# Kernel tuning notes

Measured on AMD Instinct MI355X. Metric: run time of the kernel, lower is better.

The kernel has to match this reference:

```python
import jax, jax.numpy as jnp
import numpy as np

HEADS, DH, DIM = 16, 64, 1024
GAMMA, LAMBDA_REG = 0.01, 0.001


def _ln(x, g, b, eps=1e-5):
    mu = x.mean(-1, keepdims=True)
    var = x.var(-1, keepdims=True)  # biased var, matches torch LayerNorm
    return (x - mu) / jnp.sqrt(var + eps) * g + b


def setup_inputs() -> dict:
    key = jax.random.key(0)
    ks = jax.random.split(key, 8)
    B, NQ, NK = 8, 512, 512
    inner = HEADS * DH
    rn = lambda i, shp, sc: jax.random.normal(ks[i], shp, jnp.float32) * sc
    return {
        "q": rn(0, (B, NQ, DIM), 1.0),
        "k": rn(1, (B, NK, DIM), 1.0),
        "v": rn(2, (B, NK, DIM), 1.0),
        "ln_g": jnp.ones((DIM,), jnp.float32),
        "ln_b": jnp.zeros((DIM,), jnp.float32),
        "w_in": rn(3, (DIM, inner), 0.02),
        "wp_w1": rn(4, (2 * DH, DH), 0.05),
        "wp_b1": jnp.zeros((DH,), jnp.float32),
        "wp_lng": jnp.ones((DH,), jnp.float32),
        "wp_lnb": jnp.zeros((DH,), jnp.float32),
        "wp_w2": rn(5, (DH, DH // 2), 0.05),
        "wp_b2": jnp.zeros((DH // 2,), jnp.float32),
        "wp_w3": rn(6, (DH // 2, 3), 0.05),
        "wp_b3": jnp.zeros((3,), jnp.float32),
        "w_temp": jnp.ones((1,), jnp.float32) * 0.8,
        "w_out": rn(7, (inner, DIM), 0.02),
        "b_out": jnp.zeros((DIM,), jnp.float32),
    }


def reference(q, k, v, ln_g, ln_b, w_in, wp_w1, wp_b1, wp_lng, wp_lnb,
              wp_w2, wp_b2, wp_w3, wp_b3, w_temp, w_out, b_out):
    sg = jax.lax.stop_gradient

    def proj(x):  # input_linear (dropout=identity in eval) + head split
        y = _ln(x, ln_g, ln_b) @ w_in                      # [B,N,inner]
        B, N, _ = y.shape
        return y.reshape(B, N, HEADS, DH).transpose(2, 0, 1, 3)  # [h,B,N,d]

    f_q, f_k, f_v = proj(q), proj(k), proj(v)
    m = f_k.shape[2]
    eps = 1e-8

    # --- cosine component (clamp applied twice, as in source) ---
    dots = jnp.einsum('hbnd,hbmd->hbnm', f_q, f_k)
    n1 = jnp.linalg.norm(f_q, axis=-1, keepdims=True) + eps   # [h,B,Nq,1]
    n2 = jnp.linalg.norm(f_k, axis=-1, keepdims=True) + eps   # [h,B,Nk,1]
    cosine_sim = jnp.clip(dots / (n1 * jnp.swapaxes(n2, -1, -2)), -0.98, 0.98)

    # --- regularized covariance component ---
    f_kc = f_k - f_k.mean(axis=2, keepdims=True)
    f_qc = f_q - f_q.mean(axis=-1, keepdims=True)
    cov = jnp.einsum('hbnd,hbmd->hbnm', f_qc, f_kc) / (DH ** 0.5 + 1e-6)
    health = jnp.std(cov, ddof=1)
    base = LAMBDA_REG / max(m, 1)
    reg = jnp.where(health < 1e-5, base * 5.0,
                    jnp.where(health < 1e-3, base * 2.0, base))
    cov = jnp.clip(reg * cov, -25.0, 25.0)

    # --- margin-based variance component (eval: adaptive_gamma = gamma) ---
    fqn = f_q / jnp.maximum(jnp.linalg.norm(f_q, axis=-1, keepdims=True), 1e-6)
    fkn = f_k / jnp.maximum(jnp.linalg.norm(f_k, axis=-1, keepdims=True), 1e-6)
    cs = jnp.clip(jnp.einsum('hbnd,hbmd->hbnm', fqn, fkn), -0.98, 0.98)
    margin = jnp.clip(GAMMA - cs, 0.0, 5.0)
    var_c = jnp.broadcast_to(margin.mean(-1, keepdims=True), cs.shape)

    # --- dynamic per-head weight predictor MLP ---
    qk = jnp.concatenate([f_q.mean(axis=(1, 2)), f_k.mean(axis=(1, 2))], -1)  # [h,2d]
    h1 = jax.nn.relu(_ln(qk @ wp_w1 + wp_b1, wp_lng, wp_lnb))
    h2 = jax.nn.relu(h1 @ wp_w2 + wp_b2)
    logits = jax.nn.softmax(h2 @ wp_w3 + wp_b3, -1)  # MLP ends in Softmax
    temp = jnp.clip(w_temp, 0.1, 5.0)
    w = jax.nn.softmax(logits / temp, -1)            # second softmax with temp
    w = jnp.clip(w, 0.08, 0.75)
    w = w / w.sum(-1, keepdims=True)
    cw = w[:, 0].reshape(HEADS, 1, 1, 1)
    covw = w[:, 1].reshape(HEADS, 1, 1, 1)
    varw = w[:, 2].reshape(HEADS, 1, 1, 1)

    # --- health-based normalization (stds detached, as in source) ---
    cn = sg(jnp.std(cosine_sim, ddof=1)) + 1e-6
    covn = sg(jnp.std(cov, ddof=1)) + 1e-6
    varn = sg(jnp.std(var_c, ddof=1)) + 1e-6
    ch = jnp.minimum(cn, 1.0)
    covh = jnp.minimum(covn * 10.0, 1.0)
    varh = jnp.minimum(varn * 10.0, 1.0)
    dots_f = (cw * (cosine_sim / cn * ch)
              + covw * (cov / covn * 0.4 * covh)
              + varw * (var_c / varn * 0.4 * varh))

    # --- diversity-adaptive softmax temperature ---
    div = jnp.std(dots_f, ddof=1)
    atemp = jnp.where(div < 1e-5, 0.05, jnp.where(div < 1e-3, 0.2, 0.5 + div))
    atemp = jnp.clip(atemp, 0.05, 2.0)
    attn = jax.nn.softmax(dots_f / atemp, axis=-1)

    out = jnp.einsum('hbnm,hbmd->hbnd', attn, f_v)
    out = out.transpose(1, 2, 0, 3).reshape(q.shape[0], q.shape[1], HEADS * DH)
    return out @ w_out + b_out  # output_linear (dropout=identity)
```

## Files before the change

### kernel.cpp

```cpp
#include <hip/hip_runtime.h>
#include <math.h>

#define NHEADS 16
#define DHEAD  64
#define NDIM   1024
#define NB     8
#define NSEQ   512
#define NROWS  4096
#define NHB    128
#define NTOTD  33554432.0

typedef __bf16 bf16x8 __attribute__((ext_vector_type(8)));
typedef __bf16 bf16x4 __attribute__((ext_vector_type(4)));
typedef float  f32x4  __attribute__((ext_vector_type(4)));

#define MFMA(a,b,c) __builtin_amdgcn_mfma_f32_16x16x32_bf16(a,b,c,0,0,0)

static __device__ __forceinline__ size_t qk_off(int hbq, int n, int d){
  return ((size_t)hbq*32 + (n>>4))*1024 + (size_t)(d>>3)*128 + (size_t)(n&15)*8 + (d&7);
}

#define O_DSUMH  0
#define O_DSUME  1024
#define O_SCAL   2048
#define O_COEF   3072
#define O_W      4096
#define O_RQ1    131072
#define O_RQ2    393216
#define O_MQ     655360
#define O_QDMK   917504
#define O_RK1    1179648
#define O_RK2    1441792
#define O_KS2    1703936
#define O_MARG   1966080
#define O_RCS    2228224
#define O_RCOV   2490368
#define O_MK     2752512
#define O_QCOL   2785280
#define O_QHI    4194304
#define O_QLO    12582912
#define O_KHI    20971520
#define O_KLO    29360128
#define O_VTH    37748736
#define O_VTL    46137344
#define O_LNST   54525952
#define O_WTH    71303168
#define O_WTL    73400320
#define O_OUTH   75497472
#define O_OUTL   83886080
#define O_WOTH   92274688
#define O_WOTL   94371840

static __device__ __forceinline__ float clamp98(float x){ return fminf(fmaxf(x,-0.98f),0.98f); }

__global__ __launch_bounds__(256) void ln_stats_kernel(const float* __restrict__ q,
    const float* __restrict__ k, const float* __restrict__ v, float* __restrict__ st){
  int row = blockIdx.x, t = threadIdx.x;
  const float* x = (blockIdx.y==0) ? q : (blockIdx.y==1 ? k : v);
  float4 vv = *(const float4*)(x + (size_t)row*1024 + t*4);
  float s  = vv.x+vv.y+vv.z+vv.w;
  float ss = vv.x*vv.x+vv.y*vv.y+vv.z*vv.z+vv.w*vv.w;
  for (int off=32; off; off>>=1){ s += __shfl_down(s,off); ss += __shfl_down(ss,off); }
  __shared__ float sh[8];
  if ((t&63)==0){ sh[t>>6]=s; sh[4+(t>>6)]=ss; }
  __syncthreads();
  if (t==0){
    float S=sh[0]+sh[1]+sh[2]+sh[3], SS=sh[4]+sh[5]+sh[6]+sh[7];
    float mu = S*(1.0f/1024.0f);
    st[blockIdx.y*8192 + row*2]   = mu;
    st[blockIdx.y*8192 + row*2+1] = 1.0f/sqrtf(SS*(1.0f/1024.0f) - mu*mu + 1e-5f);
  }
}

__global__ __launch_bounds__(256) void transpose_split_kernel(const float* __restrict__ wsrc,
    __bf16* __restrict__ th, __bf16* __restrict__ tl){
  __shared__ float tile[64][65];
  int k0 = blockIdx.x*64, n0 = blockIdx.y*64;
  int t = threadIdx.x;
  int c = t&63, r4 = t>>6;
  #pragma unroll
  for (int i=0;i<16;i++){
    int kr = r4 + i*4;
    tile[kr][c] = wsrc[(size_t)(k0+kr)*1024 + n0 + c];
  }
  __syncthreads();
  #pragma unroll
  for (int i=0;i<16;i++){
    int nr = r4 + i*4;
    float v = tile[c][nr];
    __bf16 hv = (__bf16)v;
    size_t o = (size_t)(n0+nr)*1024 + k0 + c;
    th[o] = hv; tl[o] = (__bf16)(v - (float)hv);
  }
}

__global__ __launch_bounds__(256) void proj_gemm_kernel(
  const float* __restrict__ q, const float* __restrict__ k, const float* __restrict__ v,
  const float* __restrict__ lnst0,
  const float* __restrict__ gv, const float* __restrict__ bv,
  const __bf16* __restrict__ Bth, const __bf16* __restrict__ Btl,
  __bf16* __restrict__ qhi, __bf16* __restrict__ qlo,
  __bf16* __restrict__ khi, __bf16* __restrict__ klo,
  __bf16* __restrict__ vth, __bf16* __restrict__ vtl)
{
  __shared__ __bf16 Ash[128][72];
  __shared__ __bf16 Asl[128][72];
  __shared__ __bf16 Bsh[64][72];
  __shared__ __bf16 Bsl[64][72];
  int z = blockIdx.z;
  const float* X = (z==0)? q : (z==1? k : v);
  const float* lnst = lnst0 + z*8192;
  __bf16* oh = (z==0)? qhi : (z==1? khi : vth);
  __bf16* ol = (z==0)? qlo : (z==1? klo : vtl);
  int t = threadIdx.x, w = t>>6, lane = t&63, lr = lane&15, lq = lane>>4;
  int vid = blockIdx.y*16 + blockIdx.x;
  int cX = vid&7, r2 = vid>>3;
  int ytile = cX*4 + (r2>>4);
  int xtile = r2&15;
  int rbase = ytile*128;
  int cbase = xtile*64;
  int wr = w>>1, wc = w&1;
  int srow = t>>3;
  int scol = (t&7)*8;
  f32x4 acc[4][2] = {};
  for (int kt=0; kt<16; kt++){
    int k0 = kt*64;
    bf16x8 va[4], vA[4], vb[2], vB[2];
    float4 g0 = *(const float4*)(gv + k0 + scol);
    float4 g1 = *(const float4*)(gv + k0 + scol + 4);
    float4 b0 = *(const float4*)(bv + k0 + scol);
    float4 b1 = *(const float4*)(bv + k0 + scol + 4);
    #pragma unroll
    for (int r=0;r<4;r++){
      int row = rbase + r*32 + srow;
      size_t gi = (size_t)row*1024 + k0 + scol;
      float4 x0 = *(const float4*)(X + gi);
      float4 x1 = *(const float4*)(X + gi + 4);
      float mu = lnst[row*2], rs = lnst[row*2+1];
      float o[8];
      o[0]=(x0.x-mu)*rs*g0.x+b0.x; o[1]=(x0.y-mu)*rs*g0.y+b0.y;
      o[2]=(x0.z-mu)*rs*g0.z+b0.z; o[3]=(x0.w-mu)*rs*g0.w+b0.w;
      o[4]=(x1.x-mu)*rs*g1.x+b1.x; o[5]=(x1.y-mu)*rs*g1.y+b1.y;
      o[6]=(x1.z-mu)*rs*g1.z+b1.z; o[7]=(x1.w-mu)*rs*g1.w+b1.w;
      bf16x8 hv, lv;
      #pragma unroll
      for (int e=0;e<8;e++){
        __bf16 hb_ = (__bf16)o[e];
        hv[e] = hb_; lv[e] = (__bf16)(o[e]-(float)hb_);
      }
      va[r]=hv; vA[r]=lv;
    }
    #pragma unroll
    for (int r=0;r<2;r++){
      size_t gi = (size_t)(cbase + r*32 + srow)*1024 + k0 + scol;
      vb[r] = *(const bf16x8*)(Bth + gi);
      vB[r] = *(const bf16x8*)(Btl + gi);
    }
    #pragma unroll
    for (int r=0;r<4;r++){
      *(bf16x8*)&Ash[r*32+srow][scol] = va[r];
      *(bf16x8*)&Asl[r*32+srow][scol] = vA[r];
    }
    #pragma unroll
    for (int r=0;r<2;r++){
      *(bf16x8*)&Bsh[r*32+srow][scol] = vb[r];
      *(bf16x8*)&Bsl[r*32+srow][scol] = vB[r];
    }
    __syncthreads();
    #pragma unroll
    for (int kc=0; kc<2; kc++){
      int ko = kc*32 + lq*8;
      bf16x8 ah[4], al[4], bh[2], bl[2];
      #pragma unroll
      for (int i=0;i<4;i++){
        ah[i] = *(const bf16x8*)&Ash[wr*64 + i*16 + lr][ko];
        al[i] = *(const bf16x8*)&Asl[wr*64 + i*16 + lr][ko];
      }
      #pragma unroll
      for (int j=0;j<2;j++){
        bh[j] = *(const bf16x8*)&Bsh[wc*32 + j*16 + lr][ko];
        bl[j] = *(const bf16x8*)&Bsl[wc*32 + j*16 + lr][ko];
      }
      #pragma unroll
      for (int i=0;i<4;i++)
        #pragma unroll
        for (int j=0;j<2;j++){
          acc[i][j] = MFMA(al[i], bh[j], acc[i][j]);
          acc[i][j] = MFMA(ah[i], bl[j], acc[i][j]);
          acc[i][j] = MFMA(ah[i], bh[j], acc[i][j]);
        }
    }
    __syncthreads();
  }
  #pragma unroll
  for (int i=0;i<4;i++)
    #pragma unroll
    for (int j=0;j<2;j++)
      #pragma unroll
      for (int r=0;r<4;r++){
        int row = rbase + wr*64 + i*16 + lq*4 + r;
        int col = cbase + wc*32 + j*16 + lr;
        float val = acc[i][j][r];
        __bf16 hv = (__bf16)val;
        __bf16 lv = (__bf16)(val - (float)hv);
        int n = row & 511, b2 = row >> 9;
        int hh = col >> 6, d = col & 63;
        int hbq = hh*8 + b2;
        size_t o;
        if (z<2){
          o = qk_off(hbq, n, d);
        } else {
          o = (((size_t)hbq*4 + (d>>4))*16 + (n>>5))*512
            + (size_t)((((n>>3)&3)*16) + (d&15))*8 + (n&7);
        }
        oh[o] = hv; ol[o] = lv;
      }
}

__global__ __launch_bounds__(256) void final_gemm_kernel(
  const __bf16* __restrict__ Ah, const __bf16* __restrict__ Al,
  const __bf16* __restrict__ Bth, const __bf16* __restrict__ Btl,
  const float* __restrict__ bias, float* __restrict__ of)
{
  __shared__ __bf16 Ash[128][72];
  __shared__ __bf16 Asl[128][72];
  __shared__ __bf16 Bsh[64][72];
  __shared__ __bf16 Bsl[64][72];
  int t = threadIdx.x, w = t>>6, lane = t&63, lr = lane&15, lq = lane>>4;
  int vid = blockIdx.y*16 + blockIdx.x;
  int cX = vid&7, r2 = vid>>3;
  int ytile = cX*4 + (r2>>4);
  int xtile = r2&15;
  int rbase = ytile*128;
  int cbase = xtile*64;
  int wr = w>>1, wc = w&1;
  int srow = t>>3;
  int scol = (t&7)*8;
  f32x4 acc[4][2] = {};
  for (int kt=0; kt<16; kt++){
    int k0 = kt*64;
    bf16x8 va[4], vA[4], vb[2], vB[2];
    #pragma unroll
    for (int r=0;r<4;r++){
      size_t gi = (size_t)(rbase + r*32 + srow)*1024 + k0 + scol;
      va[r] = *(const bf16x8*)(Ah + gi);
      vA[r] = *(const bf16x8*)(Al + gi);
    }
    #pragma unroll
    for (int r=0;r<2;r++){
      size_t gi = (size_t)(cbase + r*32 + srow)*1024 + k0 + scol;
      vb[r] = *(const bf16x8*)(Bth + gi);
      vB[r] = *(const bf16x8*)(Btl + gi);
    }
    #pragma unroll
    for (int r=0;r<4;r++){
      *(bf16x8*)&Ash[r*32+srow][scol] = va[r];
      *(bf16x8*)&Asl[r*32+srow][scol] = vA[r];
    }
    #pragma unroll
    for (int r=0;r<2;r++){
      *(bf16x8*)&Bsh[r*32+srow][scol] = vb[r];
      *(bf16x8*)&Bsl[r*32+srow][scol] = vB[r];
    }
    __syncthreads();
    #pragma unroll
    for (int kc=0; kc<2; kc++){
      int ko = kc*32 + lq*8;
      bf16x8 ah[4], al[4], bh[2], bl[2];
      #pragma unroll
      for (int i=0;i<4;i++){
        ah[i] = *(const bf16x8*)&Ash[wr*64 + i*16 + lr][ko];
        al[i] = *(const bf16x8*)&Asl[wr*64 + i*16 + lr][ko];
      }
      #pragma unroll
      for (int j=0;j<2;j++){
        bh[j] = *(const bf16x8*)&Bsh[wc*32 + j*16 + lr][ko];
        bl[j] = *(const bf16x8*)&Bsl[wc*32 + j*16 + lr][ko];
      }
      #pragma unroll
      for (int i=0;i<4;i++)
        #pragma unroll
        for (int j=0;j<2;j++){
          acc[i][j] = MFMA(al[i], bh[j], acc[i][j]);
          acc[i][j] = MFMA(ah[i], bl[j], acc[i][j]);
          acc[i][j] = MFMA(ah[i], bh[j], acc[i][j]);
        }
    }
    __syncthreads();
  }
  #pragma unroll
  for (int i=0;i<4;i++)
    #pragma unroll
    for (int j=0;j<2;j++)
      #pragma unroll
      for (int r=0;r<4;r++){
        int row = rbase + wr*64 + i*16 + lq*4 + r;
        int col = cbase + wc*32 + j*16 + lr;
        of[(size_t)row*1024 + col] = acc[i][j][r] + bias[col];
      }
}

__global__ void kstats_kernel(const __bf16* __restrict__ kh, const __bf16* __restrict__ kl,
    float* __restrict__ mk, float* __restrict__ rk1, float* __restrict__ rk2, float* __restrict__ ks2){
  int hb = blockIdx.x;
  size_t base = (size_t)hb*32768;
  int t = threadIdx.x;
  __shared__ float csA[32][64];
  __shared__ float mks_lds[64];
  __shared__ float mksum_sh;
  int c2 = t&7, mg = t>>3;
  float fs[8] = {};
  for (int m=mg; m<512; m+=32){
    size_t off = base + (size_t)(m>>4)*1024 + c2*128 + (size_t)(m&15)*8;
    bf16x8 h = *(const bf16x8*)(kh+off);
    bf16x8 l = *(const bf16x8*)(kl+off);
    #pragma unroll
    for (int e=0;e<8;e++) fs[e] += (float)h[e]+(float)l[e];
  }
  #pragma unroll
  for (int e=0;e<8;e++) csA[mg][c2*8+e] = fs[e];
  __syncthreads();
  if (t<64){
    float s=0;
    #pragma unroll
    for (int g=0;g<32;g++) s += csA[g][t];
    float vv = s*(1.0f/512.0f);
    mk[hb*64+t] = vv;
    mks_lds[t] = vv;
  }
  __syncthreads();
  if (t==0){
    float s=0;
    for (int i=0;i<64;i++) s += mks_lds[i];
    mksum_sh = s;
  }
  __syncthreads();
  float mks = mksum_sh;
  int l8 = t&7, rg = t>>3;
  for (int m=rg; m<512; m+=32){
    size_t off = base + (size_t)(m>>4)*1024 + l8*128 + (size_t)(m&15)*8;
    bf16x8 h = *(const bf16x8*)(kh+off);
    bf16x8 l = *(const bf16x8*)(kl+off);
    float s=0, ss=0;
    #pragma unroll
    for (int e=0;e<8;e++){ float vv=(float)h[e]+(float)l[e]; s+=vv; ss+=vv*vv; }
    for (int o2=4;o2;o2>>=1){ s+=__shfl_xor(s,o2); ss+=__shfl_xor(ss,o2); }
    if (l8==0){
      float nk = sqrtf(ss);
      rk1[hb*512+m] = 1.0f/(nk+1e-8f);
      rk2[hb*512+m] = 1.0f/fmaxf(nk,1e-6f);
      ks2[hb*512+m] = s - mks;
    }
  }
}

__global__ void qstats_kernel(const __bf16* __restrict__ qh, const __bf16* __restrict__ ql,
    const float* __restrict__ mk, float* __restrict__ rq1, float* __restrict__ rq2,
    float* __restrict__ mq, float* __restrict__ qdotmk, float* __restrict__ qcol){
  int hb = blockIdx.x;
  size_t base = (size_t)hb*32768;
  int t = threadIdx.x;
  __shared__ float csA[32][64];
  __shared__ float mks_lds[64];
  int c2 = t&7, mg = t>>3;
  if (t<64) mks_lds[t] = mk[hb*64+t];
  float fs[8] = {};
  for (int m=mg; m<512; m+=32){
    size_t off = base + (size_t)(m>>4)*1024 + c2*128 + (size_t)(m&15)*8;
    bf16x8 h = *(const bf16x8*)(qh+off);
    bf16x8 l = *(const bf16x8*)(ql+off);
    #pragma unroll
    for (int e=0;e<8;e++) fs[e] += (float)h[e]+(float)l[e];
  }
  #pragma unroll
  for (int e=0;e<8;e++) csA[mg][c2*8+e] = fs[e];
  __syncthreads();
  if (t<64){
    float s=0;
    #pragma unroll
    for (int g=0;g<32;g++) s += csA[g][t];
    qcol[hb*64+t] = s;
  }
  int l8 = t&7, rg = t>>3;
  float mkv[8];
  #pragma unroll
  for (int e=0;e<8;e++) mkv[e] = mks_lds[l8*8+e];
  for (int n=rg; n<512; n+=32){
    size_t off = base + (size_t)(n>>4)*1024 + l8*128 + (size_t)(n&15)*8;
    bf16x8 h = *(const bf16x8*)(qh+off);
    bf16x8 l = *(const bf16x8*)(ql+off);
    float s=0, ss=0, qd=0;
    #pragma unroll
    for (int e=0;e<8;e++){
      float vv=(float)h[e]+(float)l[e];
      s+=vv; ss+=vv*vv; qd+=vv*mkv[e];
    }
    for (int o2=4;o2;o2>>=1){ s+=__shfl_xor(s,o2); ss+=__shfl_xor(ss,o2); qd+=__shfl_xor(qd,o2); }
    if (l8==0){
      float nq = sqrtf(ss);
      rq1[hb*512+n] = 1.0f/(nq+1e-8f);
      rq2[hb*512+n] = 1.0f/fmaxf(nq,1e-6f);
      mq[hb*512+n]  = s*(1.0f/64.0f);
      qdotmk[hb*512+n] = qd;
    }
  }
}

__global__ void mlp_kernel(const float* __restrict__ qcol, const float* __restrict__ mk,
   const float* __restrict__ w1, const float* __restrict__ b1, const float* __restrict__ lng,
   const float* __restrict__ lnb, const float* __restrict__ w2, const float* __restrict__ b2,
   const float* __restrict__ w3, const float* __restrict__ b3, const float* __restrict__ wtemp,
   float* __restrict__ W){
  int h = blockIdx.x;
  int j = threadIdx.x;
  __shared__ float qk[128], h1[64], h2[32];
  float sq=0, sk=0;
  #pragma unroll
  for (int b=0;b<8;b++){
    sq += qcol[(h*8+b)*64 + j];
    sk += mk[(h*8+b)*64 + j];
  }
  qk[j]    = sq*(1.0f/4096.0f);
  qk[64+j] = sk*(1.0f/8.0f);
  __syncthreads();
  float a = b1[j];
  for (int i=0;i<128;i++) a += qk[i]*w1[i*64+j];
  float s=a, ss=a*a;
  for (int off=32; off; off>>=1){ s += __shfl_xor(s,off); ss += __shfl_xor(ss,off); }
  float mu = s*(1.0f/64.0f), var = ss*(1.0f/64.0f)-mu*mu;
  float v = (a-mu)/sqrtf(var+1e-5f)*lng[j] + lnb[j];
  h1[j] = fmaxf(v, 0.0f);
  __syncthreads();
  if (j<32){
    float a2 = b2[j];
    for (int i=0;i<64;i++) a2 += h1[i]*w2[i*32+j];
    h2[j] = fmaxf(a2,0.0f);
  }
  __syncthreads();
  if (j==0){
    float l[3];
    for (int kq=0;kq<3;kq++){ float a3=b3[kq]; for(int i=0;i<32;i++) a3 += h2[i]*w3[i*3+kq]; l[kq]=a3; }
    float m = fmaxf(l[0],fmaxf(l[1],l[2]));
    float e0=expf(l[0]-m), e1=expf(l[1]-m), e2=expf(l[2]-m);
    float si = 1.0f/(e0+e1+e2);
    float temp = fminf(fmaxf(wtemp[0], 0.1f), 5.0f);
    float t0=e0*si/temp, t1=e1*si/temp, t2=e2*si/temp;
    float m2 = fmaxf(t0,fmaxf(t1,t2));
    float f0=expf(t0-m2), f1=expf(t1-m2), f2=expf(t2-m2);
    float s2i = 1.0f/(f0+f1+f2);
    float wv[3] = {f0*s2i, f1*s2i, f2*s2i};
    float wsum=0.0f;
    for (int kq=0;kq<3;kq++){ wv[kq]=fminf(fmaxf(wv[kq],0.08f),0.75f); wsum+=wv[kq]; }
    for (int kq=0;kq<3;kq++) W[h*3+kq] = wv[kq]/wsum;
  }
}

__global__ __launch_bounds__(256) void s1_mfma_kernel(
  const __bf16* __restrict__ qhp, const __bf16* __restrict__ qlp,
  const __bf16* __restrict__ khp, const __bf16* __restrict__ klp,
  const float* __restrict__ rq1, const float* __restrict__ rq2,
  const float* __restrict__ mq, const float* __restrict__ qdmk,
  const float* __restrict__ rk1, const float* __restrict__ rk2,
  const float* __restrict__ ks2,
  double* __restrict__ dsumH, float* __restrict__ margin,
  float* __restrict__ rcs, float* __restrict__ rcov)
{
  int vid = blockIdx.y*4 + blockIdx.x;
  int cX = vid&7, r2 = vid>>3;
  int hb = cX*16 + (r2>>2);
  int n0 = (r2&3)*128;
  size_t qb = (size_t)hb*32768;
  __shared__ float sm[512][3];
  __shared__ float sn[128][4];
  int t = threadIdx.x;
  for (int mm=t; mm<512; mm+=256){
    int m = hb*512 + mm;
    sm[mm][0]=rk1[m]; sm[mm][1]=rk2[m]; sm[mm][2]=ks2[m];
  }
  if (t<128){
    int n = hb*512 + n0 + t;
    sn[t][0]=rq1[n]; sn[t][1]=rq2[n]; sn[t][2]=mq[n]; sn[t][3]=qdmk[n];
  }
  __syncthreads();
  int w = t>>6, lane = t&63, lr = lane&15, lq = lane>>4;
  int nw = w*32;
  float lcs=0,lcs2=0,lcov=0,lcov2=0,lcscov=0;
  float mrow[2][4]={}, csr[2][4]={}, cvr[2][4]={};
  for (int mc=0; mc<4; mc++){
    int m0 = mc*128;
    f32x4 acc[2][8] = {};
    #pragma unroll
    for (int kc=0; kc<2; kc++){
      bf16x8 ah[2], al[2];
      #pragma unroll
      for (int i=0;i<2;i++){
        size_t off = qb + (size_t)(((n0+nw)>>4)+i)*1024 + kc*512 + (size_t)lane*8;
        ah[i] = *(const bf16x8*)(qhp + off);
        al[i] = *(const bf16x8*)(qlp + off);
      }
      #pragma unroll
      for (int j=0;j<8;j++){
        size_t off = qb + (size_t)((m0>>4)+j)*1024 + kc*512 + (size_t)lane*8;
        bf16x8 bh = *(const bf16x8*)(khp + off);
        bf16x8 bl = *(const bf16x8*)(klp + off);
        #pragma unroll
        for (int i=0;i<2;i++){
          acc[i][j] = MFMA(ah[i], bh, acc[i][j]);
          acc[i][j] = MFMA(ah[i], bl, acc[i][j]);
          acc[i][j] = MFMA(al[i], bh, acc[i][j]);
        }
      }
    }
    #pragma unroll
    for (int i=0;i<2;i++){
      float nr1[4],nr2[4],nmq[4],nqd[4];
      #pragma unroll
      for (int r=0;r<4;r++){
        int nl = nw + i*16 + lq*4 + r;
        nr1[r]=sn[nl][0]; nr2[r]=sn[nl][1]; nmq[r]=sn[nl][2]; nqd[r]=sn[nl][3];
      }
      #pragma unroll
      for (int j=0;j<8;j++){
        int ml = m0 + j*16 + lr;
        float k1=sm[ml][0], k2=sm[ml][1], ksv=sm[ml][2];
        #pragma unroll
        for (int r=0;r<4;r++){
          float dv = acc[i][j][r];
          float cs = clamp98(dv*nr1[r]*k1);
          float c2 = clamp98(dv*nr2[r]*k2);
          float mg = fminf(fmaxf(0.01f-c2,0.0f),5.0f);
          float cv = dv - nqd[r] - nmq[r]*ksv;
          lcs+=cs; lcs2+=cs*cs; lcov+=cv; lcov2+=cv*cv; lcscov+=cs*cv;
          mrow[i][r]+=mg; csr[i][r]+=cs; cvr[i][r]+=cv;
        }
      }
    }
  }
  for (int off=1; off<16; off<<=1)
    #pragma unroll
    for (int i=0;i<2;i++)
      #pragma unroll
      for (int r=0;r<4;r++){
        mrow[i][r]+=__shfl_xor(mrow[i][r],off);
        csr[i][r] +=__shfl_xor(csr[i][r],off);
        cvr[i][r]+=__shfl_xor(cvr[i][r],off);
      }
  if (lr==0){
    #pragma unroll
    for (int i=0;i<2;i++)
      #pragma unroll
      for (int r=0;r<4;r++){
        int n = hb*512 + n0 + nw + i*16 + lq*4 + r;
        margin[n] = mrow[i][r]*(1.0f/512.0f);
        rcs[n]    = csr[i][r];
        rcov[n]   = cvr[i][r];
      }
  }
  for (int off=32; off; off>>=1){
    lcs+=__shfl_xor(lcs,off); lcs2+=__shfl_xor(lcs2,off);
    lcov+=__shfl_xor(lcov,off); lcov2+=__shfl_xor(lcov2,off);
    lcscov+=__shfl_xor(lcscov,off);
  }
  __shared__ double red[4][5];
  if (lane==0){ red[w][0]=lcs; red[w][1]=lcs2; red[w][2]=lcov; red[w][3]=lcov2; red[w][4]=lcscov; }
  __syncthreads();
  if (t==0){
    int h = hb>>3;
    for (int c=0;c<5;c++)
      atomicAdd(&dsumH[h*5+c], red[0][c]+red[1][c]+red[2][c]+red[3][c]);
  }
}

__global__ void margfin_kernel(const float* __restrict__ margin, double* __restrict__ dsumE){
  double s=0, ss=0;
  for (int k2=0;k2<4;k2++){
    int idx = blockIdx.x*1024 + k2*256 + threadIdx.x;
    float v = margin[idx];
    s += v; ss += (double)v*v;
  }
  for (int off=32; off; off>>=1){ s+=__shfl_down(s,off); ss+=__shfl_down(ss,off); }
  __shared__ double sh[8];
  int t = threadIdx.x;
  if ((t&63)==0){ sh[t>>6]=s; sh[4+(t>>6)]=ss; }
  __syncthreads();
  if (t==0){
    atomicAdd(dsumE+0, sh[0]+sh[1]+sh[2]+sh[3]);
    atomicAdd(dsumE+1, sh[4]+sh[5]+sh[6]+sh[7]);
  }
}

__global__ void scalars1_kernel(const double* __restrict__ dsumH, double* __restrict__ dsumE,
                                const float* __restrict__ W, float* __restrict__ coef){
  double Scs=0,Scs2=0,Scov=0,Scov2=0;
  for (int h=0;h<16;h++){
    Scs += dsumH[h*5+0]; Scs2 += dsumH[h*5+1];
    Scov += dsumH[h*5+2]; Scov2 += dsumH[h*5+3];
  }
  double N = NTOTD;
  double cn = sqrt(fmax((Scs2-Scs*Scs/N)/(N-1.0),0.0)) + 1e-6;
  double ch = fmin(cn, 1.0);
  const double covscale = 1.0/8.000001;
  double sc_ = Scov*covscale, sc2_ = Scov2*covscale*covscale;
  double health = sqrt(fmax((sc2_-sc_*sc_/N)/(N-1.0),0.0));
  double base = 0.001/512.0;
  double reg = health<1e-5 ? base*5.0 : (health<1e-3 ? base*2.0 : base);
  double covn = reg*health + 1e-6;
  double covh = fmin(covn*10.0, 1.0);
  double vs = dsumE[0]*512.0, vs2 = dsumE[1]*512.0;
  double varn = sqrt(fmax((vs2 - vs*vs/N)/(N-1.0),0.0)) + 1e-6;
  double varh = fmin(varn*10.0, 1.0);
  double sdf=0, sdf2=0;
  for (int h=0;h<16;h++){
    double cC  = (double)W[h*3+0]*ch/cn;
    double cCv = (double)W[h*3+1]*reg*covscale*0.4*covh/covn;
    double cVr = (double)W[h*3+2]*0.4*varh/varn;
    coef[h*3+0] = (float)cC;
    coef[h*3+1] = (float)cCv;
    coef[h*3+2] = (float)cVr;
    sdf  += cC*dsumH[h*5+0] + cCv*dsumH[h*5+2];
    sdf2 += cC*cC*dsumH[h*5+1] + cCv*cCv*dsumH[h*5+3] + 2.0*cC*cCv*dsumH[h*5+4];
  }
  dsumE[2] = sdf;
  dsumE[3] = sdf2;
}

__global__ void rowfold_kernel(const float* __restrict__ margin, const float* __restrict__ rcs,
                               const float* __restrict__ rcov, const float* __restrict__ coef,
                               double* __restrict__ dsumE){
  int idx = blockIdx.x*256 + threadIdx.x;
  int h = idx >> 12;
  float cC = coef[h*3+0], cCv = coef[h*3+1], cVr = coef[h*3+2];
  float vc = cVr * margin[idx];
  double s0 = 512.0*(double)vc;
  double s1 = 2.0*(double)vc*((double)cC*(double)rcs[idx] + (double)cCv*(double)rcov[idx])
            + 512.0*(double)vc*(double)vc;
  for (int off=32; off; off>>=1){ s0+=__shfl_down(s0,off); s1+=__shfl_down(s1,off); }
  __shared__ double sh[8];
  int t = threadIdx.x;
  if ((t&63)==0){ sh[t>>6]=s0; sh[4+(t>>6)]=s1; }
  __syncthreads();
  if (t==0){
    atomicAdd(dsumE+2, sh[0]+sh[1]+sh[2]+sh[3]);
    atomicAdd(dsumE+3, sh[4]+sh[5]+sh[6]+sh[7]);
  }
}

__global__ void scalars2_kernel(const double* __restrict__ dsumE, float* __restrict__ scal){
  double N = NTOTD;
  double div = sqrt(fmax((dsumE[3]-dsumE[2]*dsumE[2]/N)/(N-1.0),0.0));
  double at = div<1e-5 ? 0.05 : (div<1e-3 ? 0.2 : 0.5+div);
  at = fmin(fmax(at,0.05),2.0);
  scal[0] = (float)(1.0/at);
}

#define PSTRIDE 536
__global__ __launch_bounds__(512) void s3_mfma_kernel(
  const __bf16* __restrict__ qhp, const __bf16* __restrict__ qlp,
  const __bf16* __restrict__ khp, const __bf16* __restrict__ klp,
  const __bf16* __restrict__ vth, const __bf16* __restrict__ vtl,
  const float* __restrict__ rq1, const float* __restrict__ mq,
  const float* __restrict__ qdmk, const float* __restrict__ rk1,
  const float* __restrict__ ks2, const float* __restrict__ margin,
  const float* __restrict__ coef, const float* __restrict__ scal,
  __bf16* __restrict__ outh, __bf16* __restrict__ outl)
{
  int vid = blockIdx.y*16 + blockIdx.x;
  int cX = vid&7, r2 = vid>>3;
  int hb = cX*16 + (r2>>4);
  int n0 = (r2&15)*32;
  int h = hb>>3, b = hb&7;
  size_t qb = (size_t)hb*32768;

  __shared__ unsigned short Plds[32][PSTRIDE];
  __shared__ float nst[32][4];
  __shared__ float mst[512][2];
  __shared__ float pmax[32][8];
  __shared__ float psum[32][8];

  int t = threadIdx.x, w = t>>6, lane = t&63, lr = lane&15, lq = lane>>4;
  if (t<32){
    int n = hb*512 + n0 + t;
    nst[t][0] = rq1[n]; nst[t][1] = mq[n]; nst[t][2] = qdmk[n];
    nst[t][3] = coef[h*3+2]*margin[n];
  }
  {
    int m = hb*512 + t;
    mst[t][0] = rk1[m]; mst[t][1] = ks2[m];
  }
  float cC = coef[h*3+0], cCv = coef[h*3+1];
  float invat = scal[0];
  __syncthreads();

  int ms0 = w*64;
  f32x4 acc[2][4] = {};
  #pragma unroll
  for (int kc=0; kc<2; kc++){
    bf16x8 qhf[2], qlf[2];
    #pragma unroll
    for (int i=0;i<2;i++){
      size_t off = qb + (size_t)((n0>>4)+i)*1024 + kc*512 + (size_t)lane*8;
      qhf[i] = *(const bf16x8*)(qhp + off);
      qlf[i] = *(const bf16x8*)(qlp + off);
    }
    #pragma unroll
    for (int j=0;j<4;j++){
      size_t off = qb + (size_t)((ms0>>4)+j)*1024 + kc*512 + (size_t)lane*8;
      bf16x8 khf = *(const bf16x8*)(khp + off);
      bf16x8 klf = *(const bf16x8*)(klp + off);
      #pragma unroll
      for (int i=0;i<2;i++){
        acc[i][j] = MFMA(qlf[i], khf, acc[i][j]);
        acc[i][j] = MFMA(qhf[i], klf, acc[i][j]);
        acc[i][j] = MFMA(qhf[i], khf, acc[i][j]);
      }
    }
  }
  float rmax[2][4];
  #pragma unroll
  for (int i=0;i<2;i++){
    float a0[4],a1[4],a2[4],a3[4];
    #pragma unroll
    for (int r=0;r<4;r++){
      int nl = i*16 + lq*4 + r;
      a0[r]=nst[nl][0]; a1[r]=nst[nl][1]; a2[r]=nst[nl][2]; a3[r]=nst[nl][3];
      rmax[i][r] = -1e30f;
    }
    #pragma unroll
    for (int j=0;j<4;j++){
      int m = ms0 + j*16 + lr;
      float k1 = mst[m][0], ksv = mst[m][1];
      #pragma unroll
      for (int r=0;r<4;r++){
        float dv = acc[i][j][r];
        float cs = clamp98(dv*a0[r]*k1);
        float covr = dv - a2[r] - a1[r]*ksv;
        float df = cC*cs + cCv*covr + a3[r];
        acc[i][j][r] = df;
        rmax[i][r] = fmaxf(rmax[i][r], df);
      }
    }
  }
  #pragma unroll
  for (int i=0;i<2;i++)
    #pragma unroll
    for (int r=0;r<4;r++)
      for (int off=1; off<16; off<<=1)
        rmax[i][r] = fmaxf(rmax[i][r], __shfl_xor(rmax[i][r], off));
  if (lr==0){
    #pragma unroll
    for (int i=0;i<2;i++)
      #pragma unroll
      for (int r=0;r<4;r++)
        pmax[i*16+lq*4+r][w] = rmax[i][r];
  }
  __syncthreads();
  float rsum[2][4] = {};
  #pragma unroll
  for (int i=0;i<2;i++){
    float Mf[4];
    #pragma unroll
    for (int r=0;r<4;r++){
      int nl = i*16+lq*4+r;
      float m0_ = fmaxf(fmaxf(pmax[nl][0],pmax[nl][1]),fmaxf(pmax[nl][2],pmax[nl][3]));
      float m1_ = fmaxf(fmaxf(pmax[nl][4],pmax[nl][5]),fmaxf(pmax[nl][6],pmax[nl][7]));
      Mf[r] = fmaxf(m0_,m1_);
    }
    #pragma unroll
    for (int j=0;j<4;j++){
      int m = ms0 + j*16 + lr;
      #pragma unroll
      for (int r=0;r<4;r++){
        float p = __expf((acc[i][j][r]-Mf[r])*invat);
        rsum[i][r] += p;
        *(__bf16*)&Plds[i*16+lq*4+r][m] = (__bf16)p;
      }
    }
  }
  #pragma unroll
  for (int i=0;i<2;i++)
    #pragma unroll
    for (int r=0;r<4;r++)
      for (int off=1; off<16; off<<=1)
        rsum[i][r] += __shfl_xor(rsum[i][r], off);
  if (lr==0){
    #pragma unroll
    for (int i=0;i<2;i++)
      #pragma unroll
      for (int r=0;r<4;r++)
        psum[i*16+lq*4+r][w] = rsum[i][r];
  }
  __syncthreads();

  int rt = (w&1)*16;
  int dtg = w>>1;
  f32x4 acc2 = {};
  for (int kc=0; kc<16; kc++){
    bf16x8 pa = *(const bf16x8*)&Plds[rt+lr][kc*32 + lq*8];
    size_t vi = (((size_t)hb*4 + dtg)*16 + kc)*512 + (size_t)lane*8;
    bf16x8 vh = *(const bf16x8*)(vth + vi);
    bf16x8 vl = *(const bf16x8*)(vtl + vi);
    acc2 = MFMA(pa, vl, acc2);
    acc2 = MFMA(pa, vh, acc2);
  }
  float rsinv[4];
  #pragma unroll
  for (int r=0;r<4;r++){
    int nl = rt + lq*4 + r;
    float s0_ = psum[nl][0]+psum[nl][1]+psum[nl][2]+psum[nl][3];
    float s1_ = psum[nl][4]+psum[nl][5]+psum[nl][6]+psum[nl][7];
    rsinv[r] = 1.0f/(s0_+s1_);
  }
  #pragma unroll
  for (int r=0;r<4;r++){
    float o = acc2[r]*rsinv[r];
    int rowg = b*512 + n0 + rt + lq*4 + r;
    int colg = h*64 + dtg*16 + lr;
    size_t oi = (size_t)rowg*1024 + colg;
    __bf16 hv = (__bf16)o;
    outh[oi] = hv;
    outl[oi] = (__bf16)(o - (float)hv);
  }
}

extern "C" void kernel_launch(void* const* d_in, const int* in_sizes, int n_in,
                              void* d_out, int out_size, void* d_ws, size_t ws_size,
                              hipStream_t stream) {
  (void)in_sizes; (void)n_in; (void)out_size; (void)ws_size;
  const float* q     = (const float*)d_in[0];
  const float* k     = (const float*)d_in[1];
  const float* v     = (const float*)d_in[2];
  const float* ln_g  = (const float*)d_in[3];
  const float* ln_b  = (const float*)d_in[4];
  const float* w_in  = (const float*)d_in[5];
  const float* wp_w1 = (const float*)d_in[6];
  const float* wp_b1 = (const float*)d_in[7];
  const float* wp_lng= (const float*)d_in[8];
  const float* wp_lnb= (const float*)d_in[9];
  const float* wp_w2 = (const float*)d_in[10];
  const float* wp_b2 = (const float*)d_in[11];
  const float* wp_w3 = (const float*)d_in[12];
  const float* wp_b3 = (const float*)d_in[13];
  const float* w_temp= (const float*)d_in[14];
  const float* w_out = (const float*)d_in[15];
  const float* b_out = (const float*)d_in[16];

  char* ws = (char*)d_ws;
  double* dsumH = (double*)(ws + O_DSUMH);
  double* dsumE = (double*)(ws + O_DSUME);
  float* scal  = (float*)(ws + O_SCAL);
  float* coef  = (float*)(ws + O_COEF);
  float* W     = (float*)(ws + O_W);
  float* rq1   = (float*)(ws + O_RQ1);
  float* rq2   = (float*)(ws + O_RQ2);
  float* mqp   = (float*)(ws + O_MQ);
  float* qdmk  = (float*)(ws + O_QDMK);
  float* rk1   = (float*)(ws + O_RK1);
  float* rk2   = (float*)(ws + O_RK2);
  float* ks2   = (float*)(ws + O_KS2);
  float* marg  = (float*)(ws + O_MARG);
  float* rcs   = (float*)(ws + O_RCS);
  float* rcov  = (float*)(ws + O_RCOV);
  float* mk    = (float*)(ws + O_MK);
  float* qcol  = (float*)(ws + O_QCOL);
  float* lnst  = (float*)(ws + O_LNST);
  __bf16* qhi  = (__bf16*)(ws + O_QHI);
  __bf16* qlo  = (__bf16*)(ws + O_QLO);
  __bf16* khi  = (__bf16*)(ws + O_KHI);
  __bf16* klo  = (__bf16*)(ws + O_KLO);
  __bf16* vth  = (__bf16*)(ws + O_VTH);
  __bf16* vtl  = (__bf16*)(ws + O_VTL);
  __bf16* wth  = (__bf16*)(ws + O_WTH);
  __bf16* wtl  = (__bf16*)(ws + O_WTL);
  __bf16* outh = (__bf16*)(ws + O_OUTH);
  __bf16* outl = (__bf16*)(ws + O_OUTL);
  __bf16* woth = (__bf16*)(ws + O_WOTH);
  __bf16* wotl = (__bf16*)(ws + O_WOTL);
  float* outf  = (float*)d_out;

  hipMemsetAsync(ws + O_DSUMH, 0, 2048, stream);

  transpose_split_kernel<<<dim3(16,16),256,0,stream>>>(w_in,  wth, wtl);
  transpose_split_kernel<<<dim3(16,16),256,0,stream>>>(w_out, woth, wotl);
  ln_stats_kernel<<<dim3(4096,3),256,0,stream>>>(q, k, v, lnst);

  proj_gemm_kernel<<<dim3(16,32,3),256,0,stream>>>(q, k, v, lnst, ln_g, ln_b, wth, wtl,
                                                   qhi, qlo, khi, klo, vth, vtl);

  kstats_kernel<<<128,256,0,stream>>>(khi, klo, mk, rk1, rk2, ks2);
  qstats_kernel<<<128,256,0,stream>>>(qhi, qlo, mk, rq1, rq2, mqp, qdmk, qcol);
  mlp_kernel<<<16,64,0,stream>>>(qcol,mk,wp_w1,wp_b1,wp_lng,wp_lnb,wp_w2,wp_b2,wp_w3,wp_b3,w_temp,W);

  s1_mfma_kernel<<<dim3(4,128),256,0,stream>>>(qhi,qlo,khi,klo,rq1,rq2,mqp,qdmk,rk1,rk2,ks2,
                                               dsumH,marg,rcs,rcov);
  margfin_kernel<<<64,256,0,stream>>>(marg, dsumE);
  scalars1_kernel<<<1,1,0,stream>>>(dsumH, dsumE, W, coef);
  rowfold_kernel<<<256,256,0,stream>>>(marg, rcs, rcov, coef, dsumE);
  scalars2_kernel<<<1,1,0,stream>>>(dsumE, scal);

  s3_mfma_kernel<<<dim3(16,128),512,0,stream>>>(qhi,qlo,khi,klo,vth,vtl,
                                                rq1,mqp,qdmk,rk1,ks2,marg,coef,scal,outh,outl);
  final_gemm_kernel<<<dim3(16,32),256,0,stream>>>(outh, outl, woth, wotl, b_out, outf);
}
```

Baseline: 352.8 us.

## Store GEMM operands in MFMA fragment layout and load directly from global

The transposed weights and the attention output are now written in a pre-tiled 16-row fragment layout, so each lane's 8-element MFMA operand is one contiguous 16-byte load. The projection GEMM drops its shared-memory B tile and reads B fragments straight from global memory. The final GEMM drops shared memory and barriers entirely. The aim is to remove LDS staging and synchronisation, at the cost of redundant global and L2 traffic across waves and no explicit prefetch. The projection kernel also gets a 4-block occupancy hint in its launch bounds.

```diff
diff --git a/kernel.cpp b/kernel.cpp
--- a/kernel.cpp
+++ b/kernel.cpp
@@ -18,6 +18,9 @@
 
 static __device__ __forceinline__ size_t qk_off(int hbq, int n, int d){
   return ((size_t)hbq*32 + (n>>4))*1024 + (size_t)(d>>3)*128 + (size_t)(n&15)*8 + (d&7);
+}
+static __device__ __forceinline__ size_t fr_off(int r, int k2, int kblocks8){
+  return ((size_t)(r>>4)*kblocks8 + (k2>>3))*128 + (size_t)(r&15)*8 + (k2&7);
 }
 
 #define O_DSUMH  0
@@ -89,12 +92,12 @@
     int nr = r4 + i*4;
     float v = tile[c][nr];
     __bf16 hv = (__bf16)v;
-    size_t o = (size_t)(n0+nr)*1024 + k0 + c;
+    size_t o = fr_off(n0+nr, k0+c, 128);
     th[o] = hv; tl[o] = (__bf16)(v - (float)hv);
   }
 }
 
-__global__ __launch_bounds__(256) void proj_gemm_kernel(
+__global__ __launch_bounds__(256,4) void proj_gemm_kernel(
   const float* __restrict__ q, const float* __restrict__ k, const float* __restrict__ v,
   const float* __restrict__ lnst0,
   const float* __restrict__ gv, const float* __restrict__ bv,
@@ -105,8 +108,6 @@
 {
   __shared__ __bf16 Ash[128][72];
   __shared__ __bf16 Asl[128][72];
-  __shared__ __bf16 Bsh[64][72];
-  __shared__ __bf16 Bsl[64][72];
   int z = blockIdx.z;
   const float* X = (z==0)? q : (z==1? k : v);
   const float* lnst = lnst0 + z*8192;
@@ -122,10 +123,11 @@
   int wr = w>>1, wc = w&1;
   int srow = t>>3;
   int scol = (t&7)*8;
+  int cb16_0 = (cbase + wc*32)>>4;
   f32x4 acc[4][2] = {};
   for (int kt=0; kt<16; kt++){
     int k0 = kt*64;
-    bf16x8 va[4], vA[4], vb[2], vB[2];
+    bf16x8 va[4], vA[4];
     float4 g0 = *(const float4*)(gv + k0 + scol);
     float4 g1 = *(const float4*)(gv + k0 + scol + 4);
     float4 b0 = *(const float4*)(bv + k0 + scol);
@@ -151,21 +153,10 @@
       va[r]=hv; vA[r]=lv;
     }
     #pragma unroll
-    for (int r=0;r<2;r++){
-      size_t gi = (size_t)(cbase + r*32 + srow)*1024 + k0 + scol;
-      vb[r] = *(const bf16x8*)(Bth + gi);
-      vB[r] = *(const bf16x8*)(Btl + gi);
-    }
-    #pragma unroll
     for (int r=0;r<4;r++){
       *(bf16x8*)&Ash[r*32+srow][scol] = va[r];
       *(bf16x8*)&Asl[r*32+srow][scol] = vA[r];
     }
-    #pragma unroll
-    for (int r=0;r<2;r++){
-      *(bf16x8*)&Bsh[r*32+srow][scol] = vb[r];
-      *(bf16x8*)&Bsl[r*32+srow][scol] = vB[r];
-    }
     __syncthreads();
     #pragma unroll
     for (int kc=0; kc<2; kc++){
@@ -178,8 +169,9 @@
       }
       #pragma unroll
       for (int j=0;j<2;j++){
-        bh[j] = *(const bf16x8*)&Bsh[wc*32 + j*16 + lr][ko];
-        bl[j] = *(const bf16x8*)&Bsl[wc*32 + j*16 + lr][ko];
+        size_t bo = ((size_t)(cb16_0+j)*128 + (k0>>3) + kc*4)*128 + (size_t)lane*8;
+        bh[j] = *(const bf16x8*)(Bth + bo);
+        bl[j] = *(const bf16x8*)(Btl + bo);
       }
       #pragma unroll
       for (int i=0;i<4;i++)
@@ -222,10 +214,6 @@
   const __bf16* __restrict__ Bth, const __bf16* __restrict__ Btl,
   const float* __restrict__ bias, float* __restrict__ of)
 {
-  __shared__ __bf16 Ash[128][72];
-  __shared__ __bf16 Asl[128][72];
-  __shared__ __bf16 Bsh[64][72];
-  __shared__ __bf16 Bsl[64][72];
   int t = threadIdx.x, w = t>>6, lane = t&63, lr = lane&15, lq = lane>>4;
   int vid = blockIdx.y*16 + blockIdx.x;
   int cX = vid&7, r2 = vid>>3;
@@ -234,59 +222,32 @@
   int rbase = ytile*128;
   int cbase = xtile*64;
   int wr = w>>1, wc = w&1;
-  int srow = t>>3;
-  int scol = (t&7)*8;
+  int rb16_0 = (rbase + wr*64)>>4;
+  int cb16_0 = (cbase + wc*32)>>4;
   f32x4 acc[4][2] = {};
-  for (int kt=0; kt<16; kt++){
-    int k0 = kt*64;
-    bf16x8 va[4], vA[4], vb[2], vB[2];
-    #pragma unroll
-    for (int r=0;r<4;r++){
-      size_t gi = (size_t)(rbase + r*32 + srow)*1024 + k0 + scol;
-      va[r] = *(const bf16x8*)(Ah + gi);
-      vA[r] = *(const bf16x8*)(Al + gi);
-    }
-    #pragma unroll
-    for (int r=0;r<2;r++){
-      size_t gi = (size_t)(cbase + r*32 + srow)*1024 + k0 + scol;
-      vb[r] = *(const bf16x8*)(Bth + gi);
-      vB[r] = *(const bf16x8*)(Btl + gi);
-    }
-    #pragma unroll
-    for (int r=0;r<4;r++){
-      *(bf16x8*)&Ash[r*32+srow][scol] = va[r];
-      *(bf16x8*)&Asl[r*32+srow][scol] = vA[r];
-    }
-    #pragma unroll
-    for (int r=0;r<2;r++){
-      *(bf16x8*)&Bsh[r*32+srow][scol] = vb[r];
-      *(bf16x8*)&Bsl[r*32+srow][scol] = vB[r];
-    }
-    __syncthreads();
-    #pragma unroll
-    for (int kc=0; kc<2; kc++){
-      int ko = kc*32 + lq*8;
-      bf16x8 ah[4], al[4], bh[2], bl[2];
-      #pragma unroll
-      for (int i=0;i<4;i++){
-        ah[i] = *(const bf16x8*)&Ash[wr*64 + i*16 + lr][ko];
-        al[i] = *(const bf16x8*)&Asl[wr*64 + i*16 + lr][ko];
-      }
+  for (int ks=0; ks<32; ks++){
+    int kb = ks*4;
+    bf16x8 ah[4], al[4], bh[2], bl[2];
+    #pragma unroll
+    for (int i=0;i<4;i++){
+      size_t ao = ((size_t)(rb16_0+i)*128 + kb)*128 + (size_t)lane*8;
+      ah[i] = *(const bf16x8*)(Ah + ao);
+      al[i] = *(const bf16x8*)(Al + ao);
+    }
+    #pragma unroll
+    for (int j=0;j<2;j++){
+      size_t bo = ((size_t)(cb16_0+j)*128 + kb)*128 + (size_t)lane*8;
+      bh[j] = *(const bf16x8*)(Bth + bo);
+      bl[j] = *(const bf16x8*)(Btl + bo);
+    }
+    #pragma unroll
+    for (int i=0;i<4;i++)
       #pragma unroll
       for (int j=0;j<2;j++){
-        bh[j] = *(const bf16x8*)&Bsh[wc*32 + j*16 + lr][ko];
-        bl[j] = *(const bf16x8*)&Bsl[wc*32 + j*16 + lr][ko];
-      }
-      #pragma unroll
-      for (int i=0;i<4;i++)
-        #pragma unroll
-        for (int j=0;j<2;j++){
-          acc[i][j] = MFMA(al[i], bh[j], acc[i][j]);
-          acc[i][j] = MFMA(ah[i], bl[j], acc[i][j]);
-          acc[i][j] = MFMA(ah[i], bh[j], acc[i][j]);
-        }
-    }
-    __syncthreads();
+        acc[i][j] = MFMA(al[i], bh[j], acc[i][j]);
+        acc[i][j] = MFMA(ah[i], bl[j], acc[i][j]);
+        acc[i][j] = MFMA(ah[i], bh[j], acc[i][j]);
+      }
   }
   #pragma unroll
   for (int i=0;i<4;i++)
@@ -815,7 +776,7 @@
     float o = acc2[r]*rsinv[r];
     int rowg = b*512 + n0 + rt + lq*4 + r;
     int colg = h*64 + dtg*16 + lr;
-    size_t oi = (size_t)rowg*1024 + colg;
+    size_t oi = fr_off(rowg, colg, 128);
     __bf16 hv = (__bf16)o;
     outh[oi] = hv;
     outl[oi] = (__bf16)(o - (float)hv);
```

New measurement: 358.0 us. No clear change (+1.5%).
